# Performance work log

Hardware: AMD Instinct MI355X
Metric: run time of the kernel (lower is better)

## Reference

```python
import jax, jax.numpy as jnp
import numpy as np

B, S, D, H = 2, 2048, 1024, 16
DH = D // H          # 64
SP = S // 2          # projected kv length (Linformer)
SCALE = float(np.sqrt(DH))


def setup_inputs() -> dict:
    key = jax.random.key(0)
    ks = jax.random.split(key, 20)
    std = 0.02
    inp = {
        "query": jax.random.normal(ks[0], (B, S, D), jnp.float32),
        "key": jax.random.normal(ks[1], (B, S, D), jnp.float32),
        "value": jax.random.normal(ks[2], (B, S, D), jnp.float32),
        "mask": jax.random.randint(ks[3], (B, 1, 1, S), 0, 2, jnp.int32),
        "Wq": jax.random.normal(ks[4], (D, D), jnp.float32) * std,
        "bq": jnp.zeros((D,), jnp.float32),
        "Wk": jax.random.normal(ks[5], (D, D), jnp.float32) * std,
        "bk": jnp.zeros((D,), jnp.float32),
        "Wv": jax.random.normal(ks[6], (D, D), jnp.float32) * std,
        "bv": jnp.zeros((D,), jnp.float32),
        "Wo": jax.random.normal(ks[7], (D, D), jnp.float32) * std,
        "bo": jnp.zeros((D,), jnp.float32),
        "WkP": jax.random.normal(ks[8], (SP, S), jnp.float32) * std,
        "bkP": jnp.zeros((SP,), jnp.float32),
        "WvP": jax.random.normal(ks[9], (SP, S), jnp.float32) * std,
        "bvP": jnp.zeros((SP,), jnp.float32),
        "apply_proj": 1,
    }
    return inp


def reference(query, key, value, mask, Wq, bq, Wk, bk, Wv, bv, Wo, bo,
              WkP, bkP, WvP, bvP, apply_proj):
    # lin_forward path (apply_proj=True); dropout_ratio=0 -> dropout is identity.
    def heads(x, W, b):  # [B,S,D] -> [B,H,S,DH]
        return (x @ W.T + b).reshape(B, S, H, DH).transpose(0, 2, 1, 3)

    Q = heads(query, Wq, bq)
    K = heads(key, Wk, bk)
    V = heads(value, Wv, bv)

    # masked_fill on transposed [B,H,DH,S] == zero out seq positions
    mseq = (mask != 0).astype(Q.dtype).transpose(0, 1, 3, 2)  # [B,1,S,1]
    Q, K, V = Q * mseq, K * mseq, V * mseq

    # Linformer seq projection S -> SP with exact GELU ('nonlin' config)
    Kp = jax.nn.gelu(jnp.einsum('bhsd,ps->bhpd', K, WkP)
                     + bkP[None, None, :, None], approximate=False)
    Vp = jax.nn.gelu(jnp.einsum('bhsd,ps->bhpd', V, WvP)
                     + bvP[None, None, :, None], approximate=False)

    score = jnp.einsum('bhsd,bhpd->bhsp', Q, Kp) / SCALE   # [B,H,S,SP]
    attn = jax.nn.softmax(score, axis=-1)
    x = jnp.einsum('bhsp,bhpd->bhsd', attn, Vp)            # [B,H,S,DH]
    x = x.transpose(0, 2, 1, 3).reshape(B, S, D)
    return x @ Wo.T + bo
```

## Files before the change

### kernel.cpp

```cpp
#include <hip/hip_runtime.h>
#include <hip/hip_bf16.h>


typedef __attribute__((ext_vector_type(4))) float  f32x4;
typedef __attribute__((ext_vector_type(8))) short  short8;
typedef __attribute__((ext_vector_type(4))) short  short4_t;
typedef __attribute__((ext_vector_type(8))) __bf16 bf16x8;
typedef unsigned short ushort_t;

#define DEV __device__ __forceinline__

constexpr int B_ = 2, S_ = 2048, D_ = 1024, H_ = 16, SP_ = 1024;
constexpr size_t M1 = 1u << 20;
constexpr size_t XQ_OFF = 0,      XK_OFF = 4*M1,  XV_OFF = 8*M1,
                 WQ_OFF = 12*M1,  WK_OFF = 13*M1, WV_OFF = 14*M1, WO_OFF = 15*M1,
                 QB_OFF = 4*M1,   KP_OFF = 0,     VPT_OFF = 2*M1,
                 WKPB_OFF = 8*M1, WVPB_OFF = 10*M1, XO_OFF = 8*M1;

DEV ushort_t f2bf(float f) {
  unsigned u = __builtin_bit_cast(unsigned, f);
  unsigned r = ((u >> 16) & 1u) + 0x7FFFu;
  return (ushort_t)((u + r) >> 16);
}
DEV bf16x8 ld8(const ushort_t* p) {
  return __builtin_bit_cast(bf16x8, *reinterpret_cast<const short8*>(p));
}
DEV f32x4 mfma16(bf16x8 a, bf16x8 b, f32x4 c) {
  return __builtin_amdgcn_mfma_f32_16x16x32_bf16(a, b, c, 0, 0, 0);
}
DEV void gload16(const ushort_t* g, ushort_t* l) {
  __builtin_amdgcn_global_load_lds(
      (const __attribute__((address_space(1))) void*)g,
      (__attribute__((address_space(3))) void*)l, 16, 0, 0);
}
DEV void cvt2048(const float* src, ushort_t* dst, int tid) {
  const size_t off = (size_t)tid * 8;
  float4 f0 = *reinterpret_cast<const float4*>(src + off);
  float4 f1 = *reinterpret_cast<const float4*>(src + off + 4);
  ushort_t t[8] = { f2bf(f0.x), f2bf(f0.y), f2bf(f0.z), f2bf(f0.w),
                    f2bf(f1.x), f2bf(f1.y), f2bf(f1.z), f2bf(f1.w) };
  *reinterpret_cast<short8*>(dst + off) = *reinterpret_cast<short8*>(t);
}

__global__ __launch_bounds__(256) void k_convert_a(
    const float* __restrict__ q, const float* __restrict__ k,
    const float* __restrict__ v, const float* __restrict__ Wq,
    const float* __restrict__ Wk, const float* __restrict__ Wv,
    const float* __restrict__ Wo, ushort_t* __restrict__ ws)
{
  int blk = blockIdx.x; const float* src; ushort_t* dst;
  if      (blk < 2048) { src = q;  dst = ws + XQ_OFF; }
  else if (blk < 4096) { src = k;  dst = ws + XK_OFF; blk -= 2048; }
  else if (blk < 6144) { src = v;  dst = ws + XV_OFF; blk -= 4096; }
  else if (blk < 6656) { src = Wq; dst = ws + WQ_OFF; blk -= 6144; }
  else if (blk < 7168) { src = Wk; dst = ws + WK_OFF; blk -= 6656; }
  else if (blk < 7680) { src = Wv; dst = ws + WV_OFF; blk -= 7168; }
  else                 { src = Wo; dst = ws + WO_OFF; blk -= 7680; }
  cvt2048(src + (size_t)blk * 2048, dst + (size_t)blk * 2048, threadIdx.x);
}

__global__ __launch_bounds__(256) void k_convert_b(
    const float* __restrict__ WkP, const float* __restrict__ WvP,
    ushort_t* __restrict__ ws)
{
  int blk = blockIdx.x; const float* src; ushort_t* dst;
  if (blk < 1024) { src = WkP; dst = ws + WKPB_OFF; }
  else            { src = WvP; dst = ws + WVPB_OFF; blk -= 1024; }
  cvt2048(src + (size_t)blk * 2048, dst + (size_t)blk * 2048, threadIdx.x);
}

template<int BIAS, int EPI, int OUTMODE>
DEV void gemmT(const ushort_t* Ap, const ushort_t* Bp, const float* bias,
               const int* mask, void* Cp, int M, int N, int K)
{
  __shared__ __align__(16) ushort_t As[64 * 32];
  __shared__ __align__(16) ushort_t Bs[128 * 32];
  const int tid = threadIdx.x;
  const int m0 = blockIdx.x * 64, n0 = blockIdx.y * 128;
  const int w = tid >> 6, lane = tid & 63, lr = lane & 15, lg = lane >> 4;
  const int wm = (w >> 1) * 32, wn = (w & 1) * 64;

  f32x4 acc[2][4];
#pragma unroll
  for (int i = 0; i < 2; ++i)
#pragma unroll
    for (int j = 0; j < 4; ++j) acc[i][j] = f32x4{0.f, 0.f, 0.f, 0.f};

  const int gr = tid >> 2, gc = (tid & 3) * 8;

  for (int k0 = 0; k0 < K; k0 += 32) {
    gload16(Ap + (size_t)(m0 + gr) * K + k0 + gc,      As + tid*8);
    gload16(Bp + (size_t)(n0 + gr) * K + k0 + gc,      Bs + tid*8);
    gload16(Bp + (size_t)(n0 + 64 + gr) * K + k0 + gc, Bs + 64*32 + tid*8);
    __syncthreads();

    bf16x8 af[2], bfv[4];
#pragma unroll
    for (int i = 0; i < 2; ++i) af[i]  = ld8(&As[(wm + i*16 + lr)*32 + 8*lg]);
#pragma unroll
    for (int j = 0; j < 4; ++j) bfv[j] = ld8(&Bs[(wn + j*16 + lr)*32 + 8*lg]);
#pragma unroll
    for (int i = 0; i < 2; ++i)
#pragma unroll
      for (int j = 0; j < 4; ++j)
        acc[i][j] = mfma16(af[i], bfv[j], acc[i][j]);
    __syncthreads();
  }

#pragma unroll
  for (int i = 0; i < 2; ++i) {
    const int mBase = m0 + wm + i*16 + 4*lg;
#pragma unroll
    for (int j = 0; j < 4; ++j) {
      const int n = n0 + wn + j*16 + lr;
      float vv[4];
#pragma unroll
      for (int r = 0; r < 4; ++r) {
        const int m = mBase + r;
        float v = acc[i][j][r];
        if (BIAS == 2) v += bias[n];
        if (BIAS == 1) v += bias[m];
        if (EPI == 1)  v = mask[m] ? v : 0.f;
        if (EPI == 2)  v = 0.5f * v * (1.f + erff(v * 0.70710678118654752f));
        vv[r] = v;
      }
      if (OUTMODE == 0) {
#pragma unroll
        for (int r = 0; r < 4; ++r)
          ((ushort_t*)Cp)[(size_t)(mBase + r) * N + n] = f2bf(vv[r]);
      } else if (OUTMODE == 1) {
#pragma unroll
        for (int r = 0; r < 4; ++r)
          ((float*)Cp)[(size_t)(mBase + r) * N + n] = vv[r];
      } else if (OUTMODE == 2) {
        const int bb = mBase >> 11;
        const int sb = mBase & (S_ - 1);
        ushort_t t4[4] = { f2bf(vv[0]), f2bf(vv[1]), f2bf(vv[2]), f2bf(vv[3]) };
        *reinterpret_cast<short4_t*>(
            (ushort_t*)Cp + ((size_t)bb * D_ + n) * S_ + sb) =
            *reinterpret_cast<short4_t*>(t4);
      } else {
        ushort_t t4[4] = { f2bf(vv[0]), f2bf(vv[1]), f2bf(vv[2]), f2bf(vv[3]) };
        *reinterpret_cast<short4_t*>(
            (ushort_t*)Cp + (size_t)n * M + mBase) =
            *reinterpret_cast<short4_t*>(t4);
      }
    }
  }
}

__global__ __launch_bounds__(256) void k_kv(
    const float* __restrict__ bk, const float* __restrict__ bv,
    const int* __restrict__ mask, const ushort_t* __restrict__ ws,
    ushort_t* __restrict__ KbT, ushort_t* __restrict__ VbT)
{
  if (blockIdx.z == 0)
    gemmT<2, 1, 2>(ws + XK_OFF, ws + WK_OFF, bk, mask, KbT, B_*S_, D_, D_);
  else
    gemmT<2, 1, 2>(ws + XV_OFF, ws + WV_OFF, bv, mask, VbT, B_*S_, D_, D_);
}

__global__ __launch_bounds__(256) void k_q(
    const float* __restrict__ bq, const int* __restrict__ mask,
    const ushort_t* __restrict__ ws, ushort_t* __restrict__ Qb)
{
  gemmT<2, 1, 0>(ws + XQ_OFF, ws + WQ_OFF, bq, mask, Qb, B_*S_, D_, D_);
}

__global__ __launch_bounds__(256) void k_linproj(
    const float* __restrict__ bkP, const float* __restrict__ bvP,
    const ushort_t* __restrict__ ws, const ushort_t* __restrict__ KbT,
    const ushort_t* __restrict__ VbT, ushort_t* __restrict__ Kp,
    ushort_t* __restrict__ VpT)
{
  const int z = blockIdx.z, b = z >> 1, isv = z & 1;
  if (isv) {
    gemmT<1, 2, 3>(ws + WVPB_OFF, VbT + (size_t)b * D_ * S_, bvP,
                   nullptr, VpT + (size_t)b * D_ * SP_, SP_, D_, S_);
  } else {
    gemmT<1, 2, 0>(ws + WKPB_OFF, KbT + (size_t)b * D_ * S_, bkP,
                   nullptr, Kp + (size_t)b * SP_ * D_, SP_, D_, S_);
  }
}

__global__ __launch_bounds__(256) void k_outproj(
    const ushort_t* __restrict__ Xo, const ushort_t* __restrict__ Wob,
    const float* __restrict__ bo, float* __restrict__ out)
{
  gemmT<2, 0, 1>(Xo, Wob, bo, nullptr, out, B_*S_, D_, D_);
}

__global__ __launch_bounds__(512) void attn_kernel(
    const ushort_t* __restrict__ Qb, const ushort_t* __restrict__ Kp,
    const ushort_t* __restrict__ VpT, ushort_t* __restrict__ Xo)
{
  __shared__ __align__(16) ushort_t Ks[2][64 * 64];
  __shared__ __align__(16) ushort_t Vs[2][64 * 64];
  __shared__ __align__(16) ushort_t Pl[8][16][72];

  const int b = blockIdx.z, h = blockIdx.y, s0 = blockIdx.x * 128;
  const int tid = threadIdx.x, w = tid >> 6, lane = tid & 63;
  const int lr = lane & 15, lg = lane >> 4;

  const ushort_t* qp = Qb + (size_t)(b * S_ + s0 + w*16 + lr) * D_ + h * 64;
  const bf16x8 aq0 = ld8(qp + 8*lg);
  const bf16x8 aq1 = ld8(qp + 32 + 8*lg);

  const ushort_t* kbase = Kp  + (size_t)b * SP_ * D_ + h * 64;
  const ushort_t* vbase = VpT + (size_t)b * D_ * SP_ + (size_t)(h*64) * SP_;

  const int srow = tid >> 3, sch = tid & 7;
  const int schx = (sch ^ (srow & 7)) << 3;

  f32x4 o[4];
#pragma unroll
  for (int dt = 0; dt < 4; ++dt) o[dt] = f32x4{0.f, 0.f, 0.f, 0.f};
  float lsum[4] = {0.f, 0.f, 0.f, 0.f};
  constexpr float C_ = 0.18033688011112042f;

  gload16(kbase + (size_t)srow * D_ + schx, Ks[0] + tid*8);
  gload16(vbase + (size_t)srow * SP_ + schx, Vs[0] + tid*8);
  __syncthreads();

  int cur = 0;
  for (int pt = 0; pt < SP_ / 64; ++pt) {
    if (pt + 1 < SP_ / 64) {
      const int p1 = (pt + 1) * 64;
      gload16(kbase + (size_t)(p1 + srow) * D_ + schx, Ks[cur^1] + tid*8);
      gload16(vbase + (size_t)srow * SP_ + p1 + schx, Vs[cur^1] + tid*8);
    }

    const int rk7 = lr & 7;
#pragma unroll
    for (int nt = 0; nt < 4; ++nt) {
      const ushort_t* krow = Ks[cur] + (nt*16 + lr) * 64;
      f32x4 a = f32x4{0.f, 0.f, 0.f, 0.f};
      a = mfma16(aq0, ld8(krow + ((lg       ^ rk7) << 3)), a);
      a = mfma16(aq1, ld8(krow + (((4 + lg) ^ rk7) << 3)), a);
#pragma unroll
      for (int r = 0; r < 4; ++r) {
        const float p = __builtin_exp2f(a[r] * C_);
        lsum[r] += p;
        Pl[w][4*lg + r][nt*16 + lr] =
            __builtin_bit_cast(ushort_t, __float2bfloat16(p));
      }
    }

    const bf16x8 pa0 = ld8(&Pl[w][lr][8*lg]);
    const bf16x8 pa1 = ld8(&Pl[w][lr][32 + 8*lg]);
#pragma unroll
    for (int dt = 0; dt < 4; ++dt) {
      const ushort_t* vrow = Vs[cur] + (dt*16 + lr) * 64;
      o[dt] = mfma16(pa0, ld8(vrow + ((lg       ^ rk7) << 3)), o[dt]);
      o[dt] = mfma16(pa1, ld8(vrow + (((4 + lg) ^ rk7) << 3)), o[dt]);
    }

    __syncthreads();
    cur ^= 1;
  }

#pragma unroll
  for (int r = 0; r < 4; ++r) {
#pragma unroll
    for (int off2 = 1; off2 < 16; off2 <<= 1)
      lsum[r] += __shfl_xor(lsum[r], off2, 64);
    lsum[r] = 1.f / lsum[r];
  }

#pragma unroll
  for (int dt = 0; dt < 4; ++dt)
#pragma unroll
    for (int r = 0; r < 4; ++r) {
      const int srow2 = s0 + w*16 + 4*lg + r;
      Xo[(size_t)(b * S_ + srow2) * D_ + h*64 + dt*16 + lr] =
          f2bf(o[dt][r] * lsum[r]);
    }
}

extern "C" void kernel_launch(void* const* d_in, const int* in_sizes, int n_in,
                              void* d_out, int out_size, void* d_ws, size_t ws_size,
                              hipStream_t stream)
{
  const float* q   = (const float*)d_in[0];
  const float* k   = (const float*)d_in[1];
  const float* v   = (const float*)d_in[2];
  const int*   msk = (const int*)d_in[3];
  const float* Wq  = (const float*)d_in[4];
  const float* bq  = (const float*)d_in[5];
  const float* Wk  = (const float*)d_in[6];
  const float* bk  = (const float*)d_in[7];
  const float* Wv  = (const float*)d_in[8];
  const float* bv  = (const float*)d_in[9];
  const float* Wo  = (const float*)d_in[10];
  const float* bo  = (const float*)d_in[11];
  const float* WkP = (const float*)d_in[12];
  const float* bkP = (const float*)d_in[13];
  const float* WvP = (const float*)d_in[14];
  const float* bvP = (const float*)d_in[15];

  ushort_t* ws  = (ushort_t*)d_ws;
  ushort_t* Qb  = ws + QB_OFF;
  ushort_t* Kp  = ws + KP_OFF;
  ushort_t* VpT = ws + VPT_OFF;
  ushort_t* Xo  = ws + XO_OFF;
  ushort_t* KbT = (ushort_t*)d_out;
  ushort_t* VbT = KbT + 4 * M1;

  dim3 blk(256, 1, 1);
  k_convert_a<<<dim3(8192, 1, 1), blk, 0, stream>>>(q, k, v, Wq, Wk, Wv, Wo, ws);
  k_kv     <<<dim3(B_*S_/64, D_/128, 2), blk, 0, stream>>>(bk, bv, msk, ws, KbT, VbT);
  k_q      <<<dim3(B_*S_/64, D_/128, 1), blk, 0, stream>>>(bq, msk, ws, Qb);
  k_convert_b<<<dim3(2048, 1, 1), blk, 0, stream>>>(WkP, WvP, ws);
  k_linproj<<<dim3(SP_/64,  D_/128, 4), blk, 0, stream>>>(bkP, bvP, ws, KbT, VbT, Kp, VpT);
  attn_kernel<<<dim3(S_/128, H_, B_), dim3(512,1,1), 0, stream>>>(Qb, Kp, VpT, Xo);
  k_outproj<<<dim3(B_*S_/64, D_/128, 1), blk, 0, stream>>>(Xo, ws + WO_OFF, bo, (float*)d_out);
}
```

Measured before the change: 171.2 us.

## Swizzle GEMM block order and transpose score MFMA for packed P stores

The GEMM kernel remaps its linear workgroup index with an XCD-style interleave so neighbouring tiles land on the same chiplet and share cache. In the attention kernel the score MFMA operands are swapped so each lane holds four consecutive key columns of one query row. Those four values are packed to bf16 with v_cvt_pk_bf16_f32 and written to LDS as a single 8-byte store instead of four scalar 2-byte stores. The row-sum reduction becomes a per-lane sum plus two cross-group shuffles and a broadcast, replacing four 4-step shuffle trees; this relies on the transposed layout being correct and on the remap assuming the grid size divides by 8.

```diff
diff --git a/kernel.cpp b/kernel.cpp
--- a/kernel.cpp
+++ b/kernel.cpp
@@ -5,6 +5,7 @@
 typedef __attribute__((ext_vector_type(4))) float  f32x4;
 typedef __attribute__((ext_vector_type(8))) short  short8;
 typedef __attribute__((ext_vector_type(4))) short  short4_t;
+typedef __attribute__((ext_vector_type(2))) unsigned int uint32x2;
 typedef __attribute__((ext_vector_type(8))) __bf16 bf16x8;
 typedef unsigned short ushort_t;
 
@@ -76,7 +77,12 @@
   __shared__ __align__(16) ushort_t As[64 * 32];
   __shared__ __align__(16) ushort_t Bs[128 * 32];
   const int tid = threadIdx.x;
-  const int m0 = blockIdx.x * 64, n0 = blockIdx.y * 128;
+
+  const int gx = gridDim.x, gy = gridDim.y, nwg = gx * gy;
+  int lin = blockIdx.y * gx + blockIdx.x;
+  lin = (lin & 7) * (nwg >> 3) + (lin >> 3);
+  const int m0 = (lin / gy) * 64, n0 = (lin % gy) * 128;
+
   const int w = tid >> 6, lane = tid & 63, lr = lane & 15, lg = lane >> 4;
   const int wm = (w >> 1) * 32, wn = (w & 1) * 64;
 
@@ -215,7 +221,7 @@
   f32x4 o[4];
 #pragma unroll
   for (int dt = 0; dt < 4; ++dt) o[dt] = f32x4{0.f, 0.f, 0.f, 0.f};
-  float lsum[4] = {0.f, 0.f, 0.f, 0.f};
+  float lsum4[4] = {0.f, 0.f, 0.f, 0.f};
   constexpr float C_ = 0.18033688011112042f;
 
   gload16(kbase + (size_t)srow * D_ + schx, Ks[0] + tid*8);
@@ -235,15 +241,18 @@
     for (int nt = 0; nt < 4; ++nt) {
       const ushort_t* krow = Ks[cur] + (nt*16 + lr) * 64;
       f32x4 a = f32x4{0.f, 0.f, 0.f, 0.f};
-      a = mfma16(aq0, ld8(krow + ((lg       ^ rk7) << 3)), a);
-      a = mfma16(aq1, ld8(krow + (((4 + lg) ^ rk7) << 3)), a);
-#pragma unroll
-      for (int r = 0; r < 4; ++r) {
-        const float p = __builtin_exp2f(a[r] * C_);
-        lsum[r] += p;
-        Pl[w][4*lg + r][nt*16 + lr] =
-            __builtin_bit_cast(ushort_t, __float2bfloat16(p));
-      }
+      a = mfma16(ld8(krow + ((lg       ^ rk7) << 3)), aq0, a);
+      a = mfma16(ld8(krow + (((4 + lg) ^ rk7) << 3)), aq1, a);
+      const float e0 = __builtin_exp2f(a[0] * C_);
+      const float e1 = __builtin_exp2f(a[1] * C_);
+      const float e2 = __builtin_exp2f(a[2] * C_);
+      const float e3 = __builtin_exp2f(a[3] * C_);
+      lsum4[nt] += (e0 + e1) + (e2 + e3);
+      unsigned p01, p23;
+      asm("v_cvt_pk_bf16_f32 %0, %1, %2" : "=v"(p01) : "v"(e0), "v"(e1));
+      asm("v_cvt_pk_bf16_f32 %0, %1, %2" : "=v"(p23) : "v"(e2), "v"(e3));
+      uint32x2 pw; pw[0] = p01; pw[1] = p23;
+      *reinterpret_cast<uint32x2*>(&Pl[w][lr][nt*16 + 4*lg]) = pw;
     }
 
     const bf16x8 pa0 = ld8(&Pl[w][lr][8*lg]);
@@ -259,13 +268,13 @@
     cur ^= 1;
   }
 
-#pragma unroll
-  for (int r = 0; r < 4; ++r) {
-#pragma unroll
-    for (int off2 = 1; off2 < 16; off2 <<= 1)
-      lsum[r] += __shfl_xor(lsum[r], off2, 64);
-    lsum[r] = 1.f / lsum[r];
-  }
+  float lsum = (lsum4[0] + lsum4[1]) + (lsum4[2] + lsum4[3]);
+  lsum += __shfl_xor(lsum, 16, 64);
+  lsum += __shfl_xor(lsum, 32, 64);
+  float linv[4];
+#pragma unroll
+  for (int r = 0; r < 4; ++r)
+    linv[r] = 1.f / __shfl(lsum, 4*lg + r, 64);
 
 #pragma unroll
   for (int dt = 0; dt < 4; ++dt)
@@ -273,7 +282,7 @@
     for (int r = 0; r < 4; ++r) {
       const int srow2 = s0 + w*16 + 4*lg + r;
       Xo[(size_t)(b * S_ + srow2) * D_ + h*64 + dt*16 + lr] =
-          f2bf(o[dt][r] * lsum[r]);
+          f2bf(o[dt][r] * linv[r]);
     }
 }
 
```

After: 163.7 us. 1.05x faster.
